# Performance work log

Hardware: AMD Instinct MI355X
Metric: run time of the kernel (lower is better)

The kernel has to match this reference:

```python
import jax, jax.numpy as jnp
import numpy as np

BLOCK_DIMS = [(512, 512), (512, 512), (512, 512)]
OUTPUT_SIZE = 10
BATCH = 65536
BN_EPS = 1e-5


def sign_ste(x):
    # Binarize = sign() with straight-through estimator (torch code mutates .data,
    # so autograd sees identity). Forward value is exactly jnp.sign(x).
    return x + jax.lax.stop_gradient(jnp.sign(x) - x)


def setup_inputs() -> dict:
    key = jax.random.key(0)
    ks = jax.random.split(key, 2 + 6 * len(BLOCK_DIMS) + 2)
    it = iter(ks)
    x = jax.random.normal(next(it), (BATCH, BLOCK_DIMS[0][0]), dtype=jnp.float32)
    Ws, bs, gammas, betas = [], [], [], []
    for (din, dout) in BLOCK_DIMS:
        lim = 1.0 / np.sqrt(din)
        Ws.append(jax.random.uniform(next(it), (dout, din), jnp.float32, -lim, lim))
        bs.append(jax.random.uniform(next(it), (dout,), jnp.float32, -lim, lim))
        gammas.append(jnp.ones((dout,), jnp.float32))
        betas.append(jnp.zeros((dout,), jnp.float32))
        next(it); next(it)  # burn keys for determinism symmetry
    din = BLOCK_DIMS[-1][1]
    lim = 1.0 / np.sqrt(din)
    W_out = jax.random.uniform(next(it), (OUTPUT_SIZE, din), jnp.float32, -lim, lim)
    b_out = jax.random.uniform(next(it), (OUTPUT_SIZE,), jnp.float32, -lim, lim)
    return {"x": x, "Ws": Ws, "bs": bs, "gammas": gammas, "betas": betas,
            "W_out": W_out, "b_out": b_out}


def reference(x, Ws, bs, gammas, betas, W_out, b_out):
    # x.view(-1, input_size) then Binarize(x); BinarizeLinear re-binarizes its
    # input (sign is idempotent) and binarizes its weight, keeps float bias.
    h = sign_ste(x)
    for W, b, g, be in zip(Ws, bs, gammas, betas):
        h = jnp.einsum('bi,oi->bo', sign_ste(h), sign_ste(W)) + b
        # BatchNorm1d in training mode: biased batch statistics over the batch dim
        mu = jnp.mean(h, axis=0)
        var = jnp.var(h, axis=0)
        h = (h - mu) * jax.lax.rsqrt(var + BN_EPS) * g + be
        h = jnp.clip(h, -1.0, 1.0)  # Hardtanh
    h = jnp.einsum('bi,oi->bo', sign_ste(h), sign_ste(W_out)) + b_out
    return jax.nn.log_softmax(h, axis=-1)
```

## Files before the change

kernel.cpp:

```cpp
#include <hip/hip_runtime.h>
#include <stdint.h>

typedef unsigned long long u64;
typedef unsigned int u32;

#define BATCH   65536
#define DIN     512
#define NW      8
#define NCLS    10
#define RPB     64
#define NSL     16


__device__ u64 g_bits[2][BATCH * NW];
__device__ u64 g_mask[2][BATCH * NW];
__device__ u64 g_rowflag[2][BATCH / 64];
__device__ int g_colpart[2][NSL][DIN];
__device__ int g_S1[DIN];
__device__ int g_fastflag[4];
__device__ u64 g_wbitsT[NW * DIN];
__device__ u64 g_wmaskT[NW * DIN];
__device__ int g_wz[4];
__device__ u64 g_obits[NCLS * NW];
__device__ u64 g_omask[NCLS * NW];

__global__ __launch_bounds__(512) void k_init(
    const float* __restrict__ g0, const float* __restrict__ b0,
    const float* __restrict__ g1, const float* __restrict__ b1,
    const float* __restrict__ g2, const float* __restrict__ b2,
    const float* __restrict__ Wout)
{
    const int tid = threadIdx.x, bx = blockIdx.x;
    const int t = bx * 512 + tid;
    for (int k = t; k < NSL * DIN; k += 12 * 512)
        ((int*)g_colpart)[k] = 0;
    if (t < BATCH / 64) g_rowflag[0][t] = 0;
    if (t < 4) g_wz[t] = 0;

    if (bx >= 8 && bx <= 10) {
        const float* gp = (bx == 8) ? g0 : (bx == 9) ? g1 : g2;
        const float* bp = (bx == 8) ? b0 : (bx == 9) ? b1 : b2;
        __shared__ int s_ok;
        if (tid == 0) s_ok = 1;
        __syncthreads();
        float g = gp[tid], be = bp[tid];
        bool ok = (g > 0.0f) && (be == 0.0f);
        u64 bal = __ballot(ok);
        if ((tid & 63) == 0 && bal != ~0ull) s_ok = 0;
        __syncthreads();
        if (tid == 0) g_fastflag[bx - 8] = s_ok;
    }
    if (bx == 11 && tid < 128) {
        const int lane = tid & 63, wv = tid >> 6;
        for (int row = wv; row < NCLS; row += 2) {
            const float4* p = (const float4*)(Wout + (size_t)row * DIN + lane * 8);
            float4 v0 = p[0], v1 = p[1];
            float f[8] = {v0.x, v0.y, v0.z, v0.w, v1.x, v1.y, v1.z, v1.w};
            u32 byteS = 0, byteM = 0;
#pragma unroll
            for (int j = 0; j < 8; j++) {
                u32 pos = f[j] > 0.0f;
                u32 nz  = f[j] != 0.0f;
                byteS |= pos << j;
                byteM |= nz << j;
            }
            u64 wS = 0, wM = 0;
            const int src = (lane & 7) * 8;
#pragma unroll
            for (int j = 0; j < 8; j++) {
                wS |= (u64)(__shfl((int)byteS, src + j) & 0xFF) << (8 * j);
                wM |= (u64)(__shfl((int)byteM, src + j) & 0xFF) << (8 * j);
            }
            if (lane < 8) {
                g_obits[row * NW + lane] = wS;
                g_omask[row * NW + lane] = wM;
            }
        }
    }
}

__global__ __launch_bounds__(256) void k_binarize_x(const float* __restrict__ x)
{
    __shared__ int csB[DIN];
    const int tid = threadIdx.x;
    for (int i = tid; i < DIN; i += 256) csB[i] = 0;
    __syncthreads();
    const int lane = tid & 63, wave = tid >> 6;
    const int gw = blockIdx.x * 4 + wave;
    const int nwv = gridDim.x * 4;
    int cs[8];
#pragma unroll
    for (int j = 0; j < 8; j++) cs[j] = 0;

    auto proc = [&](int row, float4 v0, float4 v1) {
        float f[8] = {v0.x, v0.y, v0.z, v0.w, v1.x, v1.y, v1.z, v1.w};
        u32 byteS = 0, byteM = 0;
#pragma unroll
        for (int j = 0; j < 8; j++) {
            u32 pos = f[j] > 0.0f;
            u32 nz  = f[j] != 0.0f;
            byteS |= pos << j;
            byteM |= nz << j;
            cs[j] += nz ? (pos ? 1 : -1) : 0;
        }
        u64 wS = 0, wM = 0;
        const int src = (lane & 7) * 8;
#pragma unroll
        for (int j = 0; j < 8; j++) {
            wS |= (u64)(__shfl((int)byteS, src + j) & 0xFF) << (8 * j);
            wM |= (u64)(__shfl((int)byteM, src + j) & 0xFF) << (8 * j);
        }
        u64 ok = __ballot(byteM == 0xFFu);
        if (lane < 8)
            g_bits[0][(size_t)row * NW + lane] = wS;
        if (ok != ~0ull) {
            if (lane < 8) g_mask[0][(size_t)row * NW + lane] = wM;
            if (lane == 0)
                atomicOr(&g_rowflag[0][row >> 6], 1ull << (row & 63));
        }
    };

    for (int row = gw; row < BATCH; row += 2 * nwv) {
        const int rowB = row + nwv;
        const float4* pA = (const float4*)(x + (size_t)row  * DIN + lane * 8);
        const float4* pB = (const float4*)(x + (size_t)rowB * DIN + lane * 8);
        float4 a0 = pA[0], a1 = pA[1];
        float4 b0 = pB[0], b1 = pB[1];
        proc(row,  a0, a1);
        proc(rowB, b0, b1);
    }
#pragma unroll
    for (int j = 0; j < 8; j++)
        if (cs[j]) atomicAdd(&csB[lane * 8 + j], cs[j]);
    __syncthreads();
    for (int i = tid; i < DIN; i += 256) {
        int v = csB[i];
        if (v) atomicAdd(&g_colpart[0][blockIdx.x & (NSL - 1)][i], v);
    }
}

__global__ __launch_bounds__(512) void k_prep_w(const float* __restrict__ W,
                                                int sel, int layer)
{
    const int so = sel ^ 1;
    __shared__ int csL[DIN];
    const int tid = threadIdx.x;
    const int t1 = blockIdx.x * 512 + tid;
    if (t1 < NSL * DIN) ((int*)&g_colpart[so][0][0])[t1] = 0;
    if (t1 < BATCH / 64) g_rowflag[so][t1] = 0;
    {
        int s = 0;
#pragma unroll
        for (int p = 0; p < NSL; p++) s += g_colpart[sel][p][tid];
        csL[tid] = s;
    }
    __syncthreads();
    const int lane = tid & 63, wave = tid >> 6;
    const int gw = blockIdx.x * 8 + wave;
    const int nwv = gridDim.x * 8;
    for (int row = gw; row < DIN; row += nwv) {
        const float4* p = (const float4*)(W + (size_t)row * DIN + lane * 8);
        float4 v0 = p[0], v1 = p[1];
        float f[8] = {v0.x, v0.y, v0.z, v0.w, v1.x, v1.y, v1.z, v1.w};
        u32 byteS = 0, byteM = 0;
        int contrib = 0;
#pragma unroll
        for (int j = 0; j < 8; j++) {
            u32 pos = f[j] > 0.0f;
            u32 nz  = f[j] != 0.0f;
            byteS |= pos << j;
            byteM |= nz << j;
            int s = nz ? (pos ? 1 : -1) : 0;
            contrib += s * csL[lane * 8 + j];
        }
        u64 wS = 0, wM = 0;
        const int src = (lane & 7) * 8;
#pragma unroll
        for (int j = 0; j < 8; j++) {
            wS |= (u64)(__shfl((int)byteS, src + j) & 0xFF) << (8 * j);
            wM |= (u64)(__shfl((int)byteM, src + j) & 0xFF) << (8 * j);
        }
        if (lane < 8) {
            g_wbitsT[(size_t)lane * DIN + row] = wS;
            g_wmaskT[(size_t)lane * DIN + row] = wM;
        }
        u64 ok = __ballot(byteM == 0xFFu);
#pragma unroll
        for (int o = 32; o; o >>= 1) contrib += __shfl_down(contrib, o);
        if (lane == 0) {
            g_S1[row] = contrib;
            if (ok != ~0ull) atomicOr(&g_wz[layer], 1);
        }
    }
}

template<int FINAL>
__global__ __launch_bounds__(256, 4) void k_bingemm(int sel, int layer,
        const float* __restrict__ gamma, const float* __restrict__ beta,
        const float* __restrict__ bout, float* __restrict__ out)
{
    const int so = sel ^ 1;
    __shared__ alignas(16) u64 AT[RPB * NW];
    __shared__ u64 AZ[FINAL ? 1 : 4];
    __shared__ u64 SB[FINAL ? RPB * 9 : 1];
    __shared__ u64 SM[FINAL ? RPB * 9 : 1];
    __shared__ float ZR[FINAL ? RPB * 11 : 1];
    const int tid  = threadIdx.x;
    const int lane = tid & 63;
    const int wv   = tid >> 6;
    const int rowBase = blockIdx.x * RPB;

    {
        ulonglong2* dst = (ulonglong2*)AT;
        const ulonglong2* src = (const ulonglong2*)&g_bits[sel][(size_t)rowBase * NW];
        dst[tid] = src[tid];
    }
    const int col0 = wv * 128 + lane;
    const int col1 = col0 + 64;
    u64 w0[8], w1[8];
#pragma unroll
    for (int c = 0; c < 8; c++) {
        w0[c] = g_wbitsT[c * DIN + col0];
        w1[c] = g_wbitsT[c * DIN + col1];
    }
    const int thr0 = g_S1[col0];
    const int thr1 = g_S1[col1];
    const int R0 = (DIN << 16) - thr0, R1 = (DIN << 16) - thr1;
    const int tg0 = (R0 + ((1 << 17) - 1)) >> 17, tl0 = (R0 >> 17) + 1;
    const int tg1 = (R1 + ((1 << 17) - 1)) >> 17, tl1 = (R1 >> 17) + 1;
    const u64 rflags = g_rowflag[sel][blockIdx.x];
    const bool slowAll = (g_fastflag[layer] == 0) || (g_wz[layer] != 0);
    int cs0 = 0, cs1 = 0;
    u64 mB0 = 0, mB1 = 0, mM0 = 0, mM1 = 0;
    u64 anyz = 0;
    __syncthreads();

    if (!slowAll && rflags == 0) {
#pragma unroll 4
        for (int r = 0; r < RPB; r++) {
            const ulonglong2* Av = (const ulonglong2*)(AT + r * NW);
            ulonglong2 A0 = Av[0], A1 = Av[1], A2 = Av[2], A3 = Av[3];
            const u64 aw[8] = {A0.x, A0.y, A1.x, A1.y, A2.x, A2.y, A3.x, A3.y};
            int P0 = 0, P1 = 0;
#pragma unroll
            for (int c = 0; c < 8; c++) {
                P0 += __popcll(aw[c] ^ w0[c]);
                P1 += __popcll(aw[c] ^ w1[c]);
            }
            bool gb0 = P0 < tg0, lb0 = P0 >= tl0;
            bool gb1 = P1 < tg1, lb1 = P1 >= tl1;
            u64 gt0 = __ballot(gb0), nz0 = gt0 | __ballot(lb0);
            u64 gt1 = __ballot(gb1), nz1 = gt1 | __ballot(lb1);
            cs0 += (int)gb0 - (int)lb0;
            cs1 += (int)gb1 - (int)lb1;
            bool mine = (lane == r);
            mB0 = mine ? gt0 : mB0;  mB1 = mine ? gt1 : mB1;
            mM0 = mine ? nz0 : mM0;  mM1 = mine ? nz1 : mM1;
            if ((nz0 & nz1) != ~0ull) {
                anyz |= 1ull << r;
                if (lane == 0)
                    atomicOr(&g_rowflag[so][(rowBase + r) >> 6],
                             1ull << ((rowBase + r) & 63));
            }
        }
    } else {
        double td0 = 0.0, td1 = 0.0;
        int md0 = 0, md1 = 0;
        {
            float g = gamma[col0], be = beta[col0];
            int S1v = thr0;
            td0 = (double)S1v;
            if (g != 0.0f) {
                md0 = (g > 0.0f) ? 0 : 1;
                if (be != 0.0f) {
                    double s = rsqrt((double)DIN + 1e-5);
                    td0 = (double)S1v - 65536.0 * (double)be / (s * (double)g);
                }
            } else md0 = (be > 0.0f) ? 2 : ((be < 0.0f) ? 3 : 4);
            g = gamma[col1]; be = beta[col1]; S1v = thr1;
            td1 = (double)S1v;
            if (g != 0.0f) {
                md1 = (g > 0.0f) ? 0 : 1;
                if (be != 0.0f) {
                    double s = rsqrt((double)DIN + 1e-5);
                    td1 = (double)S1v - 65536.0 * (double)be / (s * (double)g);
                }
            } else md1 = (be > 0.0f) ? 2 : ((be < 0.0f) ? 3 : 4);
        }
        for (int r = 0; r < RPB; r++) {
            const bool fl = (rflags >> r) & 1;
            int bit0, bit1;
            if (!slowAll && !fl) {
                int P0 = 0, P1 = 0;
#pragma unroll
                for (int c = 0; c < 8; c++) {
                    u64 a = AT[r * NW + c];
                    P0 += __popcll(a ^ w0[c]);
                    P1 += __popcll(a ^ w1[c]);
                }
                int v0 = (DIN - 2 * P0) << 16;
                int v1 = (DIN - 2 * P1) << 16;
                bit0 = (v0 > thr0) - (v0 < thr0);
                bit1 = (v1 > thr1) - (v1 < thr1);
            } else {
                const int row = rowBase + r;
                int P0 = 0, Q0 = 0, P1 = 0, Q1 = 0;
#pragma unroll
                for (int c = 0; c < 8; c++) {
                    u64 a  = AT[r * NW + c];
                    u64 am = fl ? g_mask[sel][(size_t)row * NW + c] : ~0ull;
                    u64 m0 = am & g_wmaskT[c * DIN + col0];
                    u64 m1 = am & g_wmaskT[c * DIN + col1];
                    P0 += __popcll((a ^ w0[c]) & m0);  Q0 += __popcll(m0);
                    P1 += __popcll((a ^ w1[c]) & m1);  Q1 += __popcll(m1);
                }
                double Ds0 = (double)(Q0 - 2 * P0) * 65536.0;
                double Ds1 = (double)(Q1 - 2 * P1) * 65536.0;
                int c0 = (Ds0 > td0) ? 1 : ((Ds0 < td0) ? -1 : 0);
                int c1 = (Ds1 > td1) ? 1 : ((Ds1 < td1) ? -1 : 0);
                bit0 = (md0 == 0) ? c0 : (md0 == 1) ? -c0
                     : (md0 == 2) ? 1 : (md0 == 3) ? -1 : 0;
                bit1 = (md1 == 0) ? c1 : (md1 == 1) ? -c1
                     : (md1 == 2) ? 1 : (md1 == 3) ? -1 : 0;
            }
            u64 gt0 = __ballot(bit0 > 0), nz0 = __ballot(bit0 != 0);
            u64 gt1 = __ballot(bit1 > 0), nz1 = __ballot(bit1 != 0);
            cs0 += bit0;
            cs1 += bit1;
            bool mine = (lane == r);
            mB0 = mine ? gt0 : mB0;  mB1 = mine ? gt1 : mB1;
            mM0 = mine ? nz0 : mM0;  mM1 = mine ? nz1 : mM1;
            if ((nz0 & nz1) != ~0ull) {
                anyz |= 1ull << r;
                if (lane == 0)
                    atomicOr(&g_rowflag[so][(rowBase + r) >> 6],
                             1ull << ((rowBase + r) & 63));
            }
        }
    }

    if constexpr (FINAL) {
        SB[lane * 9 + 2 * wv]     = mB0;
        SB[lane * 9 + 2 * wv + 1] = mB1;
        SM[lane * 9 + 2 * wv]     = mM0;
        SM[lane * 9 + 2 * wv + 1] = mM1;
        __syncthreads();
        u64 b[NW], m[NW];
#pragma unroll
        for (int c = 0; c < NW; c++) { b[c] = SB[lane * 9 + c]; m[c] = SM[lane * 9 + c]; }
        const int cls0 = (wv < 2) ? wv * 3 : 2 + wv * 2;
        const int ncl  = (wv < 2) ? 3 : 2;
        for (int k = 0; k < ncl; k++) {
            const int o = cls0 + k;
            int P = 0, P2 = 0;
#pragma unroll
            for (int c = 0; c < NW; c++) {
                u64 om = g_omask[o * NW + c];
                u64 mm = m[c] & om;
                P  += __popcll((b[c] ^ g_obits[o * NW + c]) & mm);
                P2 += __popcll(mm);
            }
            ZR[lane * 11 + o] = (float)(P2 - 2 * P) + bout[o];
        }
        __syncthreads();
        if (wv == 0) {
            float z[NCLS], mx = -1e30f;
#pragma unroll
            for (int o = 0; o < NCLS; o++) { z[o] = ZR[lane * 11 + o]; mx = fmaxf(mx, z[o]); }
            float s = 0.0f;
#pragma unroll
            for (int o = 0; o < NCLS; o++) s += expf(z[o] - mx);
            float l = logf(s);
            float2* o2 = (float2*)(out + (size_t)(rowBase + lane) * NCLS);
#pragma unroll
            for (int p = 0; p < 5; p++) {
                float2 v;
                v.x = z[2 * p]     - mx - l;
                v.y = z[2 * p + 1] - mx - l;
                o2[p] = v;
            }
        }
    } else {
        AZ[wv] = anyz;
        __syncthreads();
        const u64 rowz = AZ[0] | AZ[1] | AZ[2] | AZ[3];
        size_t bofs = (size_t)(rowBase + lane) * NW + 2 * wv;
        ulonglong2 vb; vb.x = mB0; vb.y = mB1;
        *(ulonglong2*)&g_bits[so][bofs] = vb;
        if ((rowz >> lane) & 1) {
            ulonglong2 vm; vm.x = mM0; vm.y = mM1;
            *(ulonglong2*)&g_mask[so][bofs] = vm;
        }
        atomicAdd(&g_colpart[so][blockIdx.x & (NSL - 1)][col0], cs0);
        atomicAdd(&g_colpart[so][blockIdx.x & (NSL - 1)][col1], cs1);
    }
}

extern "C" void kernel_launch(void* const* d_in, const int* in_sizes, int n_in,
                              void* d_out, int out_size, void* d_ws, size_t ws_size,
                              hipStream_t stream)
{
    const float *x = 0, *Wl[3] = {0,0,0}, *gl[3] = {0,0,0}, *bl[3] = {0,0,0};
    const float *Wout = 0, *bout = 0;
    {
        int i = 0;
        x = (const float*)d_in[i++];
        if (i < n_in && in_sizes[i] == 3 * DIN * DIN) {
            for (int l = 0; l < 3; l++) Wl[l] = (const float*)d_in[i] + (size_t)l * DIN * DIN;
            i++;
        } else {
            for (int l = 0; l < 3 && i < n_in; l++) Wl[l] = (const float*)d_in[i++];
        }
        if (i < n_in && in_sizes[i] == 3 * DIN) i++;
        else i += 3;
        if (i < n_in && in_sizes[i] == 3 * DIN) {
            for (int l = 0; l < 3; l++) gl[l] = (const float*)d_in[i] + (size_t)l * DIN;
            i++;
        } else {
            for (int l = 0; l < 3 && i < n_in; l++) gl[l] = (const float*)d_in[i++];
        }
        if (i < n_in && in_sizes[i] == 3 * DIN) {
            for (int l = 0; l < 3; l++) bl[l] = (const float*)d_in[i] + (size_t)l * DIN;
            i++;
        } else {
            for (int l = 0; l < 3 && i < n_in; l++) bl[l] = (const float*)d_in[i++];
        }
        if (i < n_in) Wout = (const float*)d_in[i++];
        if (i < n_in) bout = (const float*)d_in[i++];
    }
    float* out = (float*)d_out;
    (void)out_size; (void)d_ws; (void)ws_size;

    k_init<<<12, 512, 0, stream>>>(gl[0], bl[0], gl[1], bl[1], gl[2], bl[2], Wout);
    k_binarize_x<<<1024, 256, 0, stream>>>(x);
    for (int l = 0; l < 2; l++) {
        int sel = l & 1;
        k_prep_w<<<64, 512, 0, stream>>>(Wl[l], sel, l);
        k_bingemm<0><<<BATCH / RPB, 256, 0, stream>>>(sel, l, gl[l], bl[l], bout, out);
    }
    k_prep_w<<<64, 512, 0, stream>>>(Wl[2], 0, 2);
    k_bingemm<1><<<BATCH / RPB, 256, 0, stream>>>(0, 2, gl[2], bl[2], bout, out);
}
```

Baseline: 360.0 us.

## Binarize all weights up front and fuse weight prep into the x-binarize kernel

All three hidden-layer weight matrices and the output weights are now binarized once, inside the same launch that binarizes x, and stored in per-layer bit buffers. The per-layer prep kernel shrinks to a threshold kernel that reads the packed bits and dots them with column sums. The x pass now gives each block a contiguous 64-row range, so the row-zero flag word is written once per block instead of by per-row atomics. This aims to cut per-layer float weight reads and launch overhead, at the cost of a larger fused kernel and extra weight storage.

```diff
diff --git a/kernel.cpp b/kernel.cpp
--- a/kernel.cpp
+++ b/kernel.cpp
@@ -15,84 +15,113 @@
 __device__ u64 g_bits[2][BATCH * NW];
 __device__ u64 g_mask[2][BATCH * NW];
 __device__ u64 g_rowflag[2][BATCH / 64];
-__device__ int g_colpart[2][NSL][DIN];
+__device__ int g_cp0[NSL * DIN + 4];
+__device__ int g_cp1[NSL * DIN];
 __device__ int g_S1[DIN];
 __device__ int g_fastflag[4];
-__device__ u64 g_wbitsT[NW * DIN];
-__device__ u64 g_wmaskT[NW * DIN];
-__device__ int g_wz[4];
+__device__ u64 g_wbitsT3[3][NW * DIN];
+__device__ u64 g_wmaskT3[3][NW * DIN];
 __device__ u64 g_obits[NCLS * NW];
 __device__ u64 g_omask[NCLS * NW];
 
-__global__ __launch_bounds__(512) void k_init(
+__device__ __forceinline__ int* cpbase(int sel) { return sel ? g_cp1 : g_cp0; }
+#define WZ_OFF (NSL * DIN)
+
+__global__ __launch_bounds__(512) void k_zero()
+{
+    const int t = blockIdx.x * 512 + threadIdx.x;
+    for (int k = t; k < NSL * DIN + 4; k += 16 * 512)
+        g_cp0[k] = 0;
+}
+
+__global__ __launch_bounds__(256) void k_prep_all(
+    const float* __restrict__ x,
+    const float* __restrict__ W0, const float* __restrict__ W1,
+    const float* __restrict__ W2,
     const float* __restrict__ g0, const float* __restrict__ b0,
     const float* __restrict__ g1, const float* __restrict__ b1,
     const float* __restrict__ g2, const float* __restrict__ b2,
     const float* __restrict__ Wout)
 {
-    const int tid = threadIdx.x, bx = blockIdx.x;
-    const int t = bx * 512 + tid;
-    for (int k = t; k < NSL * DIN; k += 12 * 512)
-        ((int*)g_colpart)[k] = 0;
-    if (t < BATCH / 64) g_rowflag[0][t] = 0;
-    if (t < 4) g_wz[t] = 0;
-
-    if (bx >= 8 && bx <= 10) {
-        const float* gp = (bx == 8) ? g0 : (bx == 9) ? g1 : g2;
-        const float* bp = (bx == 8) ? b0 : (bx == 9) ? b1 : b2;
-        __shared__ int s_ok;
-        if (tid == 0) s_ok = 1;
-        __syncthreads();
-        float g = gp[tid], be = bp[tid];
-        bool ok = (g > 0.0f) && (be == 0.0f);
-        u64 bal = __ballot(ok);
-        if ((tid & 63) == 0 && bal != ~0ull) s_ok = 0;
-        __syncthreads();
-        if (tid == 0) g_fastflag[bx - 8] = s_ok;
-    }
-    if (bx == 11 && tid < 128) {
-        const int lane = tid & 63, wv = tid >> 6;
-        for (int row = wv; row < NCLS; row += 2) {
-            const float4* p = (const float4*)(Wout + (size_t)row * DIN + lane * 8);
-            float4 v0 = p[0], v1 = p[1];
-            float f[8] = {v0.x, v0.y, v0.z, v0.w, v1.x, v1.y, v1.z, v1.w};
-            u32 byteS = 0, byteM = 0;
-#pragma unroll
-            for (int j = 0; j < 8; j++) {
-                u32 pos = f[j] > 0.0f;
-                u32 nz  = f[j] != 0.0f;
-                byteS |= pos << j;
-                byteM |= nz << j;
-            }
-            u64 wS = 0, wM = 0;
-            const int src = (lane & 7) * 8;
-#pragma unroll
-            for (int j = 0; j < 8; j++) {
-                wS |= (u64)(__shfl((int)byteS, src + j) & 0xFF) << (8 * j);
-                wM |= (u64)(__shfl((int)byteM, src + j) & 0xFF) << (8 * j);
-            }
-            if (lane < 8) {
-                g_obits[row * NW + lane] = wS;
-                g_omask[row * NW + lane] = wM;
-            }
-        }
-    }
-}
-
-__global__ __launch_bounds__(256) void k_binarize_x(const float* __restrict__ x)
-{
     __shared__ int csB[DIN];
-    const int tid = threadIdx.x;
+    __shared__ u64 AZ[4];
+    const int tid = threadIdx.x, lane = tid & 63, wv = tid >> 6;
+    const int b = blockIdx.x;
+    const int gwave = b * 4 + wv;
+
+    if (gwave < 3 * DIN) {
+        const int layer = gwave >> 9, row = gwave & (DIN - 1);
+        const float* W = (layer == 0) ? W0 : (layer == 1) ? W1 : W2;
+        const float4* p = (const float4*)(W + (size_t)row * DIN + lane * 8);
+        float4 v0 = p[0], v1 = p[1];
+        float f[8] = {v0.x, v0.y, v0.z, v0.w, v1.x, v1.y, v1.z, v1.w};
+        u32 byteS = 0, byteM = 0;
+#pragma unroll
+        for (int j = 0; j < 8; j++) {
+            u32 pos = f[j] > 0.0f;
+            u32 nz  = f[j] != 0.0f;
+            byteS |= pos << j;
+            byteM |= nz << j;
+        }
+        u64 wS = 0, wM = 0;
+        const int src = (lane & 7) * 8;
+#pragma unroll
+        for (int j = 0; j < 8; j++) {
+            wS |= (u64)(__shfl((int)byteS, src + j) & 0xFF) << (8 * j);
+            wM |= (u64)(__shfl((int)byteM, src + j) & 0xFF) << (8 * j);
+        }
+        if (lane < 8) {
+            g_wbitsT3[layer][(size_t)lane * DIN + row] = wS;
+            g_wmaskT3[layer][(size_t)lane * DIN + row] = wM;
+        }
+        u64 ok = __ballot(byteM == 0xFFu);
+        if (lane == 0 && ok != ~0ull) atomicOr(&g_cp0[WZ_OFF + layer], 1);
+    } else if (gwave < 3 * DIN + NCLS) {
+        const int row = gwave - 3 * DIN;
+        const float4* p = (const float4*)(Wout + (size_t)row * DIN + lane * 8);
+        float4 v0 = p[0], v1 = p[1];
+        float f[8] = {v0.x, v0.y, v0.z, v0.w, v1.x, v1.y, v1.z, v1.w};
+        u32 byteS = 0, byteM = 0;
+#pragma unroll
+        for (int j = 0; j < 8; j++) {
+            u32 pos = f[j] > 0.0f;
+            u32 nz  = f[j] != 0.0f;
+            byteS |= pos << j;
+            byteM |= nz << j;
+        }
+        u64 wS = 0, wM = 0;
+        const int src = (lane & 7) * 8;
+#pragma unroll
+        for (int j = 0; j < 8; j++) {
+            wS |= (u64)(__shfl((int)byteS, src + j) & 0xFF) << (8 * j);
+            wM |= (u64)(__shfl((int)byteM, src + j) & 0xFF) << (8 * j);
+        }
+        if (lane < 8) {
+            g_obits[row * NW + lane] = wS;
+            g_omask[row * NW + lane] = wM;
+        }
+    } else if (gwave < 3 * DIN + NCLS + 3) {
+        const int layer = gwave - (3 * DIN + NCLS);
+        const float* gp = (layer == 0) ? g0 : (layer == 1) ? g1 : g2;
+        const float* bp = (layer == 0) ? b0 : (layer == 1) ? b1 : b2;
+        bool allok = true;
+#pragma unroll
+        for (int j = 0; j < 8; j++) {
+            float gv = gp[j * 64 + lane], bv = bp[j * 64 + lane];
+            allok &= (__ballot((gv > 0.0f) && (bv == 0.0f)) == ~0ull);
+        }
+        if (lane == 0) g_fastflag[layer] = allok ? 1 : 0;
+    }
+
     for (int i = tid; i < DIN; i += 256) csB[i] = 0;
     __syncthreads();
-    const int lane = tid & 63, wave = tid >> 6;
-    const int gw = blockIdx.x * 4 + wave;
-    const int nwv = gridDim.x * 4;
     int cs[8];
 #pragma unroll
     for (int j = 0; j < 8; j++) cs[j] = 0;
-
-    auto proc = [&](int row, float4 v0, float4 v1) {
+    u64 zb = 0;
+    const int rbase = b * 64 + wv * 16;
+
+    auto proc = [&](int row, int rb, float4 v0, float4 v1) {
         float f[8] = {v0.x, v0.y, v0.z, v0.w, v1.x, v1.y, v1.z, v1.w};
         u32 byteS = 0, byteM = 0;
 #pragma unroll
@@ -115,83 +144,71 @@
             g_bits[0][(size_t)row * NW + lane] = wS;
         if (ok != ~0ull) {
             if (lane < 8) g_mask[0][(size_t)row * NW + lane] = wM;
-            if (lane == 0)
-                atomicOr(&g_rowflag[0][row >> 6], 1ull << (row & 63));
+            zb |= 1ull << rb;
         }
     };
 
-    for (int row = gw; row < BATCH; row += 2 * nwv) {
-        const int rowB = row + nwv;
-        const float4* pA = (const float4*)(x + (size_t)row  * DIN + lane * 8);
+    for (int k = 0; k < 16; k += 2) {
+        const int rowA = rbase + k, rowB = rowA + 1;
+        const float4* pA = (const float4*)(x + (size_t)rowA * DIN + lane * 8);
         const float4* pB = (const float4*)(x + (size_t)rowB * DIN + lane * 8);
         float4 a0 = pA[0], a1 = pA[1];
-        float4 b0 = pB[0], b1 = pB[1];
-        proc(row,  a0, a1);
-        proc(rowB, b0, b1);
+        float4 c0 = pB[0], c1 = pB[1];
+        proc(rowA, wv * 16 + k,     a0, a1);
+        proc(rowB, wv * 16 + k + 1, c0, c1);
     }
 #pragma unroll
     for (int j = 0; j < 8; j++)
         if (cs[j]) atomicAdd(&csB[lane * 8 + j], cs[j]);
+    if (lane == 0) AZ[wv] = zb;
     __syncthreads();
+    if (tid == 0) g_rowflag[0][b] = AZ[0] | AZ[1] | AZ[2] | AZ[3];
     for (int i = tid; i < DIN; i += 256) {
         int v = csB[i];
-        if (v) atomicAdd(&g_colpart[0][blockIdx.x & (NSL - 1)][i], v);
+        if (v) atomicAdd(&g_cp0[(b & (NSL - 1)) * DIN + i], v);
     }
 }
 
-__global__ __launch_bounds__(512) void k_prep_w(const float* __restrict__ W,
-                                                int sel, int layer)
+__global__ __launch_bounds__(512) void k_s1(int sel, int layer)
 {
     const int so = sel ^ 1;
     __shared__ int csL[DIN];
     const int tid = threadIdx.x;
     const int t1 = blockIdx.x * 512 + tid;
-    if (t1 < NSL * DIN) ((int*)&g_colpart[so][0][0])[t1] = 0;
-    if (t1 < BATCH / 64) g_rowflag[so][t1] = 0;
     {
+        int* cpn = cpbase(so);
+        if (t1 < NSL * DIN) cpn[t1] = 0;
+        if (t1 < BATCH / 64) g_rowflag[so][t1] = 0;
+    }
+    {
+        const int* cps = cpbase(sel);
         int s = 0;
 #pragma unroll
-        for (int p = 0; p < NSL; p++) s += g_colpart[sel][p][tid];
+        for (int p = 0; p < NSL; p++) s += cps[p * DIN + tid];
         csL[tid] = s;
     }
     __syncthreads();
-    const int lane = tid & 63, wave = tid >> 6;
-    const int gw = blockIdx.x * 8 + wave;
-    const int nwv = gridDim.x * 8;
-    for (int row = gw; row < DIN; row += nwv) {
-        const float4* p = (const float4*)(W + (size_t)row * DIN + lane * 8);
-        float4 v0 = p[0], v1 = p[1];
-        float f[8] = {v0.x, v0.y, v0.z, v0.w, v1.x, v1.y, v1.z, v1.w};
-        u32 byteS = 0, byteM = 0;
-        int contrib = 0;
-#pragma unroll
-        for (int j = 0; j < 8; j++) {
-            u32 pos = f[j] > 0.0f;
-            u32 nz  = f[j] != 0.0f;
-            byteS |= pos << j;
-            byteM |= nz << j;
-            int s = nz ? (pos ? 1 : -1) : 0;
-            contrib += s * csL[lane * 8 + j];
-        }
-        u64 wS = 0, wM = 0;
-        const int src = (lane & 7) * 8;
-#pragma unroll
-        for (int j = 0; j < 8; j++) {
-            wS |= (u64)(__shfl((int)byteS, src + j) & 0xFF) << (8 * j);
-            wM |= (u64)(__shfl((int)byteM, src + j) & 0xFF) << (8 * j);
-        }
-        if (lane < 8) {
-            g_wbitsT[(size_t)lane * DIN + row] = wS;
-            g_wmaskT[(size_t)lane * DIN + row] = wM;
-        }
-        u64 ok = __ballot(byteM == 0xFFu);
-#pragma unroll
-        for (int o = 32; o; o >>= 1) contrib += __shfl_down(contrib, o);
-        if (lane == 0) {
-            g_S1[row] = contrib;
-            if (ok != ~0ull) atomicOr(&g_wz[layer], 1);
-        }
-    }
+    const int lane = tid & 63, wv = tid >> 6;
+    const int row = blockIdx.x * 8 + wv;
+    u64 wS_h = 0, wM_h = 0;
+    if (lane < 8) {
+        wS_h = g_wbitsT3[layer][(size_t)lane * DIN + row];
+        wM_h = g_wmaskT3[layer][(size_t)lane * DIN + row];
+    }
+    const u64 wS = __shfl(wS_h, lane >> 3);
+    const u64 wM = __shfl(wM_h, lane >> 3);
+    const u32 s8 = (u32)(wS >> (8 * (lane & 7))) & 0xFF;
+    const u32 m8 = (u32)(wM >> (8 * (lane & 7))) & 0xFF;
+    int acc = 0;
+#pragma unroll
+    for (int k = 0; k < 8; k++) {
+        int c = csL[lane * 8 + k];
+        int v = ((s8 >> k) & 1) ? c : -c;
+        acc += ((m8 >> k) & 1) ? v : 0;
+    }
+#pragma unroll
+    for (int o = 32; o; o >>= 1) acc += __shfl_down(acc, o);
+    if (lane == 0) g_S1[row] = acc;
 }
 
 template<int FINAL>
@@ -209,6 +226,9 @@
     const int lane = tid & 63;
     const int wv   = tid >> 6;
     const int rowBase = blockIdx.x * RPB;
+    const u64* wbT = g_wbitsT3[layer];
+    const u64* wmT = g_wmaskT3[layer];
+    int* cpo = cpbase(so);
 
     {
         ulonglong2* dst = (ulonglong2*)AT;
@@ -220,8 +240,8 @@
     u64 w0[8], w1[8];
 #pragma unroll
     for (int c = 0; c < 8; c++) {
-        w0[c] = g_wbitsT[c * DIN + col0];
-        w1[c] = g_wbitsT[c * DIN + col1];
+        w0[c] = wbT[c * DIN + col0];
+        w1[c] = wbT[c * DIN + col1];
     }
     const int thr0 = g_S1[col0];
     const int thr1 = g_S1[col1];
@@ -229,7 +249,7 @@
     const int tg0 = (R0 + ((1 << 17) - 1)) >> 17, tl0 = (R0 >> 17) + 1;
     const int tg1 = (R1 + ((1 << 17) - 1)) >> 17, tl1 = (R1 >> 17) + 1;
     const u64 rflags = g_rowflag[sel][blockIdx.x];
-    const bool slowAll = (g_fastflag[layer] == 0) || (g_wz[layer] != 0);
+    const bool slowAll = (g_fastflag[layer] == 0) || (g_cp0[WZ_OFF + layer] != 0);
     int cs0 = 0, cs1 = 0;
     u64 mB0 = 0, mB1 = 0, mM0 = 0, mM1 = 0;
     u64 anyz = 0;
@@ -309,8 +329,8 @@
                 for (int c = 0; c < 8; c++) {
                     u64 a  = AT[r * NW + c];
                     u64 am = fl ? g_mask[sel][(size_t)row * NW + c] : ~0ull;
-                    u64 m0 = am & g_wmaskT[c * DIN + col0];
-                    u64 m1 = am & g_wmaskT[c * DIN + col1];
+                    u64 m0 = am & wmT[c * DIN + col0];
+                    u64 m1 = am & wmT[c * DIN + col1];
                     P0 += __popcll((a ^ w0[c]) & m0);  Q0 += __popcll(m0);
                     P1 += __popcll((a ^ w1[c]) & m1);  Q1 += __popcll(m1);
                 }
@@ -391,8 +411,8 @@
             ulonglong2 vm; vm.x = mM0; vm.y = mM1;
             *(ulonglong2*)&g_mask[so][bofs] = vm;
         }
-        atomicAdd(&g_colpart[so][blockIdx.x & (NSL - 1)][col0], cs0);
-        atomicAdd(&g_colpart[so][blockIdx.x & (NSL - 1)][col1], cs1);
+        atomicAdd(&cpo[(blockIdx.x & (NSL - 1)) * DIN + col0], cs0);
+        atomicAdd(&cpo[(blockIdx.x & (NSL - 1)) * DIN + col1], cs1);
     }
 }
 
@@ -431,13 +451,14 @@
     float* out = (float*)d_out;
     (void)out_size; (void)d_ws; (void)ws_size;
 
-    k_init<<<12, 512, 0, stream>>>(gl[0], bl[0], gl[1], bl[1], gl[2], bl[2], Wout);
-    k_binarize_x<<<1024, 256, 0, stream>>>(x);
-    for (int l = 0; l < 2; l++) {
-        int sel = l & 1;
-        k_prep_w<<<64, 512, 0, stream>>>(Wl[l], sel, l);
-        k_bingemm<0><<<BATCH / RPB, 256, 0, stream>>>(sel, l, gl[l], bl[l], bout, out);
-    }
-    k_prep_w<<<64, 512, 0, stream>>>(Wl[2], 0, 2);
+    k_zero<<<16, 512, 0, stream>>>();
+    k_prep_all<<<1024, 256, 0, stream>>>(x, Wl[0], Wl[1], Wl[2],
+                                         gl[0], bl[0], gl[1], bl[1], gl[2], bl[2],
+                                         Wout);
+    k_s1<<<64, 512, 0, stream>>>(0, 0);
+    k_bingemm<0><<<BATCH / RPB, 256, 0, stream>>>(0, 0, gl[0], bl[0], bout, out);
+    k_s1<<<64, 512, 0, stream>>>(1, 1);
+    k_bingemm<0><<<BATCH / RPB, 256, 0, stream>>>(1, 1, gl[1], bl[1], bout, out);
+    k_s1<<<64, 512, 0, stream>>>(0, 2);
     k_bingemm<1><<<BATCH / RPB, 256, 0, stream>>>(0, 2, gl[2], bl[2], bout, out);
 }
```

Measured after the change: 353.0 us. Within noise of the previous version (-2.0%).
